# Performance work log

Measured on AMD Instinct MI355X. Metric: run time of the kernel, lower is better.

Reference implementation:

```python
import jax, jax.numpy as jnp
import numpy as np

# ForwardDiffusion config (init_kwargs)
TMIN, TMAX, DT = 0.0, 1.0, 0.001
LENGTH = 1024
BATCH = 64
THETA = 1.0      # mu(x, t) = -THETA * x   (Ornstein-Uhlenbeck drift)
SIGMA0 = 0.5     # sigma(x, t) = SIGMA0    (constant diffusion)

_TIME = jnp.asarray(np.arange(TMIN, TMAX, DT), dtype=jnp.float32)
STEPS = _TIME.shape[0]  # 1000


def setup_inputs() -> dict:
    key = jax.random.key(0)
    kx, kn = jax.random.split(key)
    x = jax.random.normal(kx, (BATCH, LENGTH), dtype=jnp.float32)
    # per-step noise vector, shape (steps-1, length); broadcast over batch like the
    # original tf.random.normal((length,))
    noise = jax.random.normal(kn, (STEPS - 1, LENGTH), dtype=jnp.float32)
    return {"x": x, "noise": noise}


def reference(x, noise):
    dt = jnp.float32(DT)
    sqrt_dt = jnp.sqrt(dt)

    def mu(x, t):
        return -THETA * x

    def sigma(x, t):
        return jnp.float32(SIGMA0)

    def step(carry, inp):
        t, z = inp  # t: scalar, z: (length,)
        x_new = carry + mu(carry, t) * dt + sigma(carry, t) * sqrt_dt * z
        return x_new, x_new

    # Euler-Maruyama scan over time steps 1..steps-1
    _, xs = jax.lax.scan(step, x, (_TIME[1:], noise))  # xs: [steps-1, batch, length]
    traj = jnp.concatenate([x[None], xs], axis=0)       # [steps, batch, length]
    return jnp.transpose(traj, (1, 0, 2))               # [batch, steps, length]
```

## Files before the change

kernel.cpp:

```cpp
#include <hip/hip_runtime.h>
#include <math.h>


namespace {
constexpr int LEN    = 1024;
constexpr int BATCH  = 64;
constexpr int STEPS  = 1000;
constexpr int NST    = 999;
constexpr int CHUNK  = 16;
constexpr int NCHUNK = (NST + CHUNK - 1) / CHUNK;
constexpr float THETA = 1.0f;
constexpr float DT    = 0.001f;
}

__global__ __launch_bounds__(1024) void k_partial(const float* __restrict__ noise,
                                                  float* __restrict__ S) {
    const int l = threadIdx.x;
    const int g = blockIdx.x;
    const float a = 1.0f - THETA * DT;
    if (g == 0) S[l] = 0.0f;
    const int t0 = g * CHUNK + 1;
    const int t1 = min((g + 1) * CHUNK, NST);
    float acc = 0.0f;
    for (int t = t0; t <= t1; ++t) {
        acc = a * acc + noise[(t - 1) * LEN + l];
        S[t * LEN + l] = acc;
    }
}

__global__ __launch_bounds__(1024) void k_combine(const float* __restrict__ S,
                                                  float* __restrict__ carry,
                                                  float* __restrict__ apow) {
    const int l = threadIdx.x;
    const float a = 1.0f - THETA * DT;
    if (l < STEPS) apow[l] = powf(a, (float)l);
    __syncthreads();
    float cr = 0.0f;
    for (int g = 0; g < NCHUNK; ++g) {
        carry[g * LEN + l] = cr;
        const int t1  = min((g + 1) * CHUNK, NST);
        const int len = t1 - g * CHUNK;
        cr = apow[len] * cr + S[t1 * LEN + l];
    }
}

__global__ __launch_bounds__(256) void k_emit(const float* __restrict__ x0,
                                              const float* __restrict__ S,
                                              const float* __restrict__ carry,
                                              const float* __restrict__ apow,
                                              float* __restrict__ out) {
    const int blk = blockIdx.x;
    const int b = blk / STEPS;
    const int t = blk - b * STEPS;
    const int g = (t - 1) / CHUNK;
    const int tloc = t - g * CHUNK;
    const float ap = apow[t];
    const float al = apow[tloc];
    const float c = 0.5f * sqrtf(DT);
    const int l4 = threadIdx.x;
    const float4 x  = ((const float4*)(x0 + b * LEN))[l4];
    const float4 s  = ((const float4*)(S + t * LEN))[l4];
    const float4 cr = ((const float4*)(carry + g * LEN))[l4];
    float4 o;
    o.x = ap * x.x + c * (s.x + al * cr.x);
    o.y = ap * x.y + c * (s.y + al * cr.y);
    o.z = ap * x.z + c * (s.z + al * cr.z);
    o.w = ap * x.w + c * (s.w + al * cr.w);
    ((float4*)(out + (size_t)blk * LEN))[l4] = o;
}

extern "C" void kernel_launch(void* const* d_in, const int* in_sizes, int n_in,
                              void* d_out, int out_size, void* d_ws, size_t ws_size,
                              hipStream_t stream) {
    const float* x     = (const float*)d_in[0];
    const float* noise = (const float*)d_in[1];
    float* out = (float*)d_out;
    float* ws  = (float*)d_ws;

    float* S     = ws;
    float* carry = S + STEPS * LEN;
    float* apow  = carry + NCHUNK * LEN;

    hipLaunchKernelGGL(k_partial, dim3(NCHUNK), dim3(1024), 0, stream, noise, S);
    hipLaunchKernelGGL(k_combine, dim3(1), dim3(1024), 0, stream, S, carry, apow);
    hipLaunchKernelGGL(k_emit, dim3(BATCH * STEPS), dim3(256), 0, stream,
                       x, S, carry, apow, out);
}
```

Before: 307.9 us.

## Parallelize the carry combine, prefetch chunk sums, use nontemporal output stores

The combine kernel is split across four 256-thread blocks. It preloads all chunk-end partial sums into registers before the serial recurrence, replacing per-step apow lookups with a constant a^16. The partial kernel is also split into 256-thread blocks. The emit kernel now uses a 2D grid, vector-type arithmetic and nontemporal stores for the large output write. The goal is to cut the latency-bound single-block combine and to reduce cache pollution from streaming the output. The hardcoded a^16 constant assumes every chunk except the last holds 16 steps.

After: 271.9 us. -11.7%, faster.

```diff
diff --git a/kernel.cpp b/kernel.cpp
--- a/kernel.cpp
+++ b/kernel.cpp
@@ -11,36 +11,44 @@
 constexpr int NCHUNK = (NST + CHUNK - 1) / CHUNK;
 constexpr float THETA = 1.0f;
 constexpr float DT    = 0.001f;
+typedef float f32x4 __attribute__((ext_vector_type(4)));
 }
 
-__global__ __launch_bounds__(1024) void k_partial(const float* __restrict__ noise,
-                                                  float* __restrict__ S) {
-    const int l = threadIdx.x;
+__global__ __launch_bounds__(256) void k_partial(const float* __restrict__ noise,
+                                                 float* __restrict__ S) {
+    const int l = blockIdx.y * 256 + threadIdx.x;
     const int g = blockIdx.x;
     const float a = 1.0f - THETA * DT;
     if (g == 0) S[l] = 0.0f;
     const int t0 = g * CHUNK + 1;
     const int t1 = min((g + 1) * CHUNK, NST);
     float acc = 0.0f;
+    #pragma unroll
     for (int t = t0; t <= t1; ++t) {
         acc = a * acc + noise[(t - 1) * LEN + l];
         S[t * LEN + l] = acc;
     }
 }
 
-__global__ __launch_bounds__(1024) void k_combine(const float* __restrict__ S,
-                                                  float* __restrict__ carry,
-                                                  float* __restrict__ apow) {
-    const int l = threadIdx.x;
+__global__ __launch_bounds__(256) void k_combine(const float* __restrict__ S,
+                                                 float* __restrict__ carry,
+                                                 float* __restrict__ apow) {
+    const int l = blockIdx.x * 256 + threadIdx.x;
     const float a = 1.0f - THETA * DT;
     if (l < STEPS) apow[l] = powf(a, (float)l);
-    __syncthreads();
+
+    float vals[NCHUNK];
+    #pragma unroll
+    for (int g = 0; g < NCHUNK; ++g) {
+        const int t1 = min((g + 1) * CHUNK, NST);
+        vals[g] = S[t1 * LEN + l];
+    }
+    const float a16 = 0.98411684f;
     float cr = 0.0f;
+    #pragma unroll
     for (int g = 0; g < NCHUNK; ++g) {
         carry[g * LEN + l] = cr;
-        const int t1  = min((g + 1) * CHUNK, NST);
-        const int len = t1 - g * CHUNK;
-        cr = apow[len] * cr + S[t1 * LEN + l];
+        cr = a16 * cr + vals[g];
     }
 }
 
@@ -49,24 +57,20 @@
                                               const float* __restrict__ carry,
                                               const float* __restrict__ apow,
                                               float* __restrict__ out) {
-    const int blk = blockIdx.x;
-    const int b = blk / STEPS;
-    const int t = blk - b * STEPS;
-    const int g = (t - 1) / CHUNK;
+    const int b = blockIdx.x;
+    const int t = blockIdx.y;
+    const int g = (max(t, 1) - 1) >> 4;
     const int tloc = t - g * CHUNK;
+    const float c  = 0.5f * sqrtf(DT);
     const float ap = apow[t];
-    const float al = apow[tloc];
-    const float c = 0.5f * sqrtf(DT);
+    const float cal = c * apow[tloc];
     const int l4 = threadIdx.x;
-    const float4 x  = ((const float4*)(x0 + b * LEN))[l4];
-    const float4 s  = ((const float4*)(S + t * LEN))[l4];
-    const float4 cr = ((const float4*)(carry + g * LEN))[l4];
-    float4 o;
-    o.x = ap * x.x + c * (s.x + al * cr.x);
-    o.y = ap * x.y + c * (s.y + al * cr.y);
-    o.z = ap * x.z + c * (s.z + al * cr.z);
-    o.w = ap * x.w + c * (s.w + al * cr.w);
-    ((float4*)(out + (size_t)blk * LEN))[l4] = o;
+    const f32x4 x  = ((const f32x4*)(x0 + b * LEN))[l4];
+    const f32x4 s  = ((const f32x4*)(S + t * LEN))[l4];
+    const f32x4 cr = ((const f32x4*)(carry + g * LEN))[l4];
+    f32x4 o = ap * x + c * s + cal * cr;
+    f32x4* dst = (f32x4*)(out + ((size_t)b * STEPS + t) * LEN) + l4;
+    __builtin_nontemporal_store(o, dst);
 }
 
 extern "C" void kernel_launch(void* const* d_in, const int* in_sizes, int n_in,
@@ -81,8 +85,8 @@
     float* carry = S + STEPS * LEN;
     float* apow  = carry + NCHUNK * LEN;
 
-    hipLaunchKernelGGL(k_partial, dim3(NCHUNK), dim3(1024), 0, stream, noise, S);
-    hipLaunchKernelGGL(k_combine, dim3(1), dim3(1024), 0, stream, S, carry, apow);
-    hipLaunchKernelGGL(k_emit, dim3(BATCH * STEPS), dim3(256), 0, stream,
+    hipLaunchKernelGGL(k_partial, dim3(NCHUNK, 4), dim3(256), 0, stream, noise, S);
+    hipLaunchKernelGGL(k_combine, dim3(4), dim3(256), 0, stream, S, carry, apow);
+    hipLaunchKernelGGL(k_emit, dim3(BATCH, STEPS), dim3(256), 0, stream,
                        x, S, carry, apow, out);
 }
```
